# Kernel tuning notes

Measured on AMD Instinct MI355X. Metric: run time of the kernel, lower is better.

## Reference

```python
import jax, jax.numpy as jnp
import numpy as np

TOPK = 20
TEMP = 1.0
B, N = 256, 50000


def _idcg_vector(topk):
    # idcg_vector[k-1] = sum_{i=0}^{k-1} 1/log2(i+2)
    return jnp.cumsum(1.0 / jnp.log2(jnp.arange(topk, dtype=jnp.float32) + 2.0))


def setup_inputs() -> dict:
    key = jax.random.key(0)
    k1, k2, k3 = jax.random.split(key, 3)
    scores_top = jax.random.normal(k1, (B, TOPK), dtype=jnp.float32)
    scores = jax.random.normal(k2, (B, N), dtype=jnp.float32)
    labels = jax.random.randint(k3, (B, TOPK), 0, 2).astype(jnp.float32)
    return {"scores_top": scores_top, "scores": scores, "labels": labels}


def reference(scores_top, scores, labels):
    # SmoothRank: rank_j = sum_i sigmoid((scores_i - scores_top_j)/temp) + 0.5
    diff = (scores[:, None, :] - scores_top[:, :, None]) / TEMP  # (B, topk, N)
    ranks = jnp.sum(jax.nn.sigmoid(diff), axis=-1) + 0.5          # (B, topk)
    d = jnp.log2(ranks + 1.0)
    dg = labels / d                                               # (B, topk)
    # dcg@p for p=1..topk is a cumulative sum (replaces the Python loop)
    dcg = jnp.cumsum(dg, axis=-1)                                 # (B, topk)
    idcg = _idcg_vector(TOPK)
    k_sum = jnp.sum(labels, axis=-1).astype(jnp.int32)            # (B,)
    p = jnp.arange(1, TOPK + 1, dtype=jnp.int32)                  # (topk,)
    k_clamped = jnp.minimum(k_sum[:, None], p[None, :])           # (B, topk)
    ndcg = dcg / idcg[k_clamped - 1]
    return ndcg
```

## Files before the change

### kernel.cpp

```cpp
#include <hip/hip_runtime.h>

#define TOPK 20
#define NITEMS 50000
#define BLOCK 1024
#define NWAVES (BLOCK / 64)

__global__ __launch_bounds__(BLOCK) void smoothdcg_kernel(
    const float* __restrict__ scores_top,
    const float* __restrict__ scores,
    const float* __restrict__ labels,
    float* __restrict__ out)
{
    const int b   = blockIdx.x;
    const int tid = threadIdx.x;

    __shared__ float s_c[TOPK];
    __shared__ float s_partial[NWAVES][TOPK];

    if (tid < TOPK) {
        s_c[tid] = __expf(scores_top[b * TOPK + tid]);
    }
    __syncthreads();

    float c[TOPK];
#pragma unroll
    for (int j = 0; j < TOPK; ++j) c[j] = s_c[j];

    float acc[TOPK];
#pragma unroll
    for (int j = 0; j < TOPK; ++j) acc[j] = 0.0f;

    const float4* row = (const float4*)(scores + (size_t)b * NITEMS);
    const int n4 = NITEMS / 4;

    for (int i = tid; i < n4; i += BLOCK) {
        float4 v = row[i];
        float e0 = __expf(-v.x);
        float e1 = __expf(-v.y);
        float e2 = __expf(-v.z);
        float e3 = __expf(-v.w);
#pragma unroll
        for (int j = 0; j < TOPK; ++j) {
            acc[j] += __builtin_amdgcn_rcpf(fmaf(c[j], e0, 1.0f));
            acc[j] += __builtin_amdgcn_rcpf(fmaf(c[j], e1, 1.0f));
            acc[j] += __builtin_amdgcn_rcpf(fmaf(c[j], e2, 1.0f));
            acc[j] += __builtin_amdgcn_rcpf(fmaf(c[j], e3, 1.0f));
        }
    }

#pragma unroll
    for (int j = 0; j < TOPK; ++j) {
        float v = acc[j];
#pragma unroll
        for (int off = 32; off >= 1; off >>= 1)
            v += __shfl_down(v, off, 64);
        acc[j] = v;
    }

    const int wave = tid >> 6;
    const int lane = tid & 63;
    if (lane == 0) {
#pragma unroll
        for (int j = 0; j < TOPK; ++j) s_partial[wave][j] = acc[j];
    }
    __syncthreads();

    if (tid == 0) {
        float rank[TOPK];
        for (int j = 0; j < TOPK; ++j) {
            float s = 0.0f;
            for (int w = 0; w < NWAVES; ++w) s += s_partial[w][j];
            rank[j] = s + 0.5f;
        }
        float idcg[TOPK];
        float run = 0.0f;
        for (int i = 0; i < TOPK; ++i) {
            run += 1.0f / log2f((float)i + 2.0f);
            idcg[i] = run;
        }
        float lab[TOPK];
        int ksum = 0;
        for (int j = 0; j < TOPK; ++j) {
            lab[j] = labels[b * TOPK + j];
            ksum += (int)(lab[j] + 0.5f);
        }
        float dcg = 0.0f;
        for (int j = 0; j < TOPK; ++j) {
            float d = log2f(rank[j] + 1.0f);
            dcg += lab[j] / d;
            int kc  = (ksum < (j + 1)) ? ksum : (j + 1);
            int idx = kc - 1;
            if (idx < 0) idx += TOPK;
            out[b * TOPK + j] = dcg / idcg[idx];
        }
    }
}

extern "C" void kernel_launch(void* const* d_in, const int* in_sizes, int n_in,
                              void* d_out, int out_size, void* d_ws, size_t ws_size,
                              hipStream_t stream) {
    const float* scores_top = (const float*)d_in[0];
    const float* scores     = (const float*)d_in[1];
    const float* labels     = (const float*)d_in[2];
    float* out              = (float*)d_out;

    const int B = in_sizes[0] / TOPK;
    smoothdcg_kernel<<<dim3(B), dim3(BLOCK), 0, stream>>>(scores_top, scores, labels, out);
}
```

Measured before the change: 114.4 us.

## Combine four sigmoids into one rational, split rows across two blocks

The four per-element reciprocals per top-k item are merged into a single rational expression built from elementary symmetric polynomials of the exp terms, so each (item, topk) group needs one rcp instead of four. Each row is now split across two blocks, with a second finalize kernel doing the reduction and the NDCG. The loop also prefetches the next float4, and the exp constants are moved to scalar registers with readfirstlane. The aim is to cut transcendental work and raise occupancy and parallelism, at the cost of an extra kernel launch and possible precision loss in the combined fraction for large exponent values.

```diff
diff --git a/kernel.cpp b/kernel.cpp
--- a/kernel.cpp
+++ b/kernel.cpp
@@ -4,57 +4,83 @@
 #define NITEMS 50000
 #define BLOCK 1024
 #define NWAVES (BLOCK / 64)
+#define SPLIT 2
+#define HALF_N (NITEMS / SPLIT)
+#define NH4 (HALF_N / 4)
 
-__global__ __launch_bounds__(BLOCK) void smoothdcg_kernel(
+__device__ __forceinline__ float readfirstlane_f32(float x) {
+    return __int_as_float(__builtin_amdgcn_readfirstlane(__float_as_int(x)));
+}
+
+__global__ __launch_bounds__(BLOCK, 8) void partial_kernel(
     const float* __restrict__ scores_top,
     const float* __restrict__ scores,
-    const float* __restrict__ labels,
-    float* __restrict__ out)
+    float* __restrict__ partials)
 {
-    const int b   = blockIdx.x;
-    const int tid = threadIdx.x;
+    const int bid  = blockIdx.x;
+    const int row  = bid >> 1;
+    const int half = bid & 1;
+    const int tid  = threadIdx.x;
 
-    __shared__ float s_c[TOPK];
     __shared__ float s_partial[NWAVES][TOPK];
 
-    if (tid < TOPK) {
-        s_c[tid] = __expf(scores_top[b * TOPK + tid]);
+    float c[TOPK], c2[TOPK];
+#pragma unroll
+    for (int j = 0; j < TOPK; ++j) {
+        float cj = readfirstlane_f32(__expf(scores_top[row * TOPK + j]));
+        c[j]  = cj;
+        c2[j] = readfirstlane_f32(cj * cj);
     }
-    __syncthreads();
-
-    float c[TOPK];
-#pragma unroll
-    for (int j = 0; j < TOPK; ++j) c[j] = s_c[j];
 
     float acc[TOPK];
 #pragma unroll
     for (int j = 0; j < TOPK; ++j) acc[j] = 0.0f;
 
-    const float4* row = (const float4*)(scores + (size_t)b * NITEMS);
-    const int n4 = NITEMS / 4;
+    const float4* rp = (const float4*)(scores + (size_t)row * NITEMS + (size_t)half * HALF_N);
 
-    for (int i = tid; i < n4; i += BLOCK) {
-        float4 v = row[i];
+    float4 v = make_float4(0.f, 0.f, 0.f, 0.f);
+    if (tid < NH4) v = rp[tid];
+
+    for (int i = tid; i < NH4; i += BLOCK) {
+        const int inext = i + BLOCK;
+        float4 vn = v;
+        if (inext < NH4) vn = rp[inext];
+
         float e0 = __expf(-v.x);
         float e1 = __expf(-v.y);
         float e2 = __expf(-v.z);
         float e3 = __expf(-v.w);
+
+        float s01 = e0 + e1, s23 = e2 + e3;
+        float p01 = e0 * e1, p23 = e2 * e3;
+        float E1 = s01 + s23;
+        float E2 = fmaf(s01, s23, p01 + p23);
+        float E3 = fmaf(p01, s23, p23 * s01);
+        float E4 = p01 * p23;
+        float F1 = 3.0f * E1;
+        float F2 = E2 + E2;
+
 #pragma unroll
         for (int j = 0; j < TOPK; ++j) {
-            acc[j] += __builtin_amdgcn_rcpf(fmaf(c[j], e0, 1.0f));
-            acc[j] += __builtin_amdgcn_rcpf(fmaf(c[j], e1, 1.0f));
-            acc[j] += __builtin_amdgcn_rcpf(fmaf(c[j], e2, 1.0f));
-            acc[j] += __builtin_amdgcn_rcpf(fmaf(c[j], e3, 1.0f));
+            float n1  = fmaf(E3, c[j], F2);
+            float n2  = fmaf(F1, c[j], 4.0f);
+            float num = fmaf(c2[j], n1, n2);
+            float d1  = fmaf(E4, c[j], E3);
+            float d2  = fmaf(d1, c[j], E2);
+            float d3  = fmaf(E1, c[j], 1.0f);
+            float den = fmaf(c2[j], d2, d3);
+            acc[j] = fmaf(num, __builtin_amdgcn_rcpf(den), acc[j]);
         }
+        v = vn;
     }
 
 #pragma unroll
     for (int j = 0; j < TOPK; ++j) {
-        float v = acc[j];
+        float r = acc[j];
 #pragma unroll
         for (int off = 32; off >= 1; off >>= 1)
-            v += __shfl_down(v, off, 64);
-        acc[j] = v;
+            r += __shfl_down(r, off, 64);
+        acc[j] = r;
     }
 
     const int wave = tid >> 6;
@@ -65,13 +91,30 @@
     }
     __syncthreads();
 
+    if (tid < TOPK) {
+        float s = 0.0f;
+#pragma unroll
+        for (int w = 0; w < NWAVES; ++w) s += s_partial[w][tid];
+        partials[bid * TOPK + tid] = s;
+    }
+}
+
+__global__ __launch_bounds__(64) void finalize_kernel(
+    const float* __restrict__ partials,
+    const float* __restrict__ labels,
+    float* __restrict__ out)
+{
+    const int b   = blockIdx.x;
+    const int tid = threadIdx.x;
+
+    __shared__ float s_rank[TOPK];
+    if (tid < TOPK) {
+        s_rank[tid] = partials[(2 * b) * TOPK + tid]
+                    + partials[(2 * b + 1) * TOPK + tid] + 0.5f;
+    }
+    __syncthreads();
+
     if (tid == 0) {
-        float rank[TOPK];
-        for (int j = 0; j < TOPK; ++j) {
-            float s = 0.0f;
-            for (int w = 0; w < NWAVES; ++w) s += s_partial[w][j];
-            rank[j] = s + 0.5f;
-        }
         float idcg[TOPK];
         float run = 0.0f;
         for (int i = 0; i < TOPK; ++i) {
@@ -86,7 +129,7 @@
         }
         float dcg = 0.0f;
         for (int j = 0; j < TOPK; ++j) {
-            float d = log2f(rank[j] + 1.0f);
+            float d = log2f(s_rank[j] + 1.0f);
             dcg += lab[j] / d;
             int kc  = (ksum < (j + 1)) ? ksum : (j + 1);
             int idx = kc - 1;
@@ -103,7 +146,9 @@
     const float* scores     = (const float*)d_in[1];
     const float* labels     = (const float*)d_in[2];
     float* out              = (float*)d_out;
+    float* partials         = (float*)d_ws;
 
     const int B = in_sizes[0] / TOPK;
-    smoothdcg_kernel<<<dim3(B), dim3(BLOCK), 0, stream>>>(scores_top, scores, labels, out);
+    partial_kernel<<<dim3(B * SPLIT), dim3(BLOCK), 0, stream>>>(scores_top, scores, partials);
+    finalize_kernel<<<dim3(B), dim3(64), 0, stream>>>(partials, labels, out);
 }
```

After: 104.1 us. 8.9% less time.
